# Performance work log

Measured on AMD Instinct MI355X. Metric: run time of the kernel, lower is better.

Reference implementation:

```python
import jax, jax.numpy as jnp
import numpy as np

B, S, D, H = 2, 2048, 2048, 16
DH = D // H  # 128


def _rope(x, cos, sin):
    # Faithful to the source: x is (B, H, S, Dh) (already transposed), and the
    # original apply_rotary_emb slices freqs_cis[:, :H, :] and broadcasts over
    # the S axis -> rotation angle depends on head index (source quirk).
    h = x.shape[1]
    c = cos[:, :h, :][:, :, None, :]  # (1, H, 1, Dh/2)
    s = sin[:, :h, :][:, :, None, :]
    half = x.shape[-1] // 2
    re, im = x[..., :half], x[..., half:]
    return jnp.concatenate([re * c - im * s, re * s + im * c], axis=-1)


def setup_inputs() -> dict:
    key = jax.random.key(0)
    k0, k1, k2 = jax.random.split(key, 3)
    x = jax.random.normal(k0, (B, S, D), jnp.float32)
    Wqkv = jax.random.normal(k1, (D, 3 * D), jnp.float32) / np.float32(np.sqrt(D))
    bqkv = jnp.zeros((3 * D,), jnp.float32)
    Wout = jax.random.normal(k2, (D, D), jnp.float32) / np.float32(np.sqrt(D))
    bout = jnp.zeros((D,), jnp.float32)
    # standard RoPE frequency table, stored as cos/sin (unit-modulus complex)
    inv_freq = 1.0 / (10000.0 ** (np.arange(0, DH // 2, dtype=np.float32) / (DH // 2)))
    ang = np.outer(np.arange(S, dtype=np.float32), inv_freq)  # (S, Dh/2)
    freqs_cos = jnp.asarray(np.cos(ang)[None], jnp.float32)   # (1, S, Dh/2)
    freqs_sin = jnp.asarray(np.sin(ang)[None], jnp.float32)
    mask = jnp.triu(jnp.ones((S, S), bool), 1)[None, None]    # causal, True = masked
    return {"x": x, "Wqkv": Wqkv, "bqkv": bqkv, "Wout": Wout, "bout": bout,
            "freqs_cos": freqs_cos, "freqs_sin": freqs_sin, "mask": mask}


def reference(x, Wqkv, bqkv, Wout, bout, freqs_cos, freqs_sin, mask):
    b, s, d = x.shape
    scale = DH ** (-0.5)
    qkv = x @ Wqkv + bqkv                                   # (B, S, 3D)
    q, k, v = jnp.split(qkv, 3, axis=-1)
    to_heads = lambda t: t.reshape(b, s, H, DH).transpose(0, 2, 1, 3)  # (B,H,S,Dh)
    q, k, v = to_heads(q), to_heads(k), to_heads(v)
    q = _rope(q, freqs_cos, freqs_sin)
    k = _rope(k, freqs_cos, freqs_sin)
    scores = jnp.einsum('bhqd,bhkd->bhqk', q, k) * scale
    scores = jnp.where(mask, -jnp.inf, scores)
    p = jax.nn.softmax(scores, axis=-1)                     # dropout p=0 (eval)
    out = jnp.einsum('bhqk,bhkd->bhqd', p, v)
    out = out.transpose(0, 2, 1, 3).reshape(b, s, d)
    return out @ Wout + bout
```

## Files before the change

kernel.cpp:

```cpp
#include <hip/hip_runtime.h>

#define S_ 2048
#define D_ 2048
#define H_ 16
#define DH_ 128

typedef __attribute__((ext_vector_type(8))) short short8;
typedef __attribute__((ext_vector_type(4))) float f32x4;
typedef __attribute__((ext_vector_type(8))) unsigned short ushort8;
typedef __attribute__((ext_vector_type(4))) unsigned short ushort4v;

__device__ __forceinline__ unsigned short f2bf(float f) {
  unsigned int u;
  __builtin_memcpy(&u, &f, 4);
  unsigned int lsb = (u >> 16) & 1u;
  u += 0x7fffu + lsb;
  return (unsigned short)(u >> 16);
}

__device__ __forceinline__ void gload_lds16(const void* g, void* l) {
  __builtin_amdgcn_global_load_lds(
      (const __attribute__((address_space(1))) unsigned int*)g,
      (__attribute__((address_space(3))) unsigned int*)l, 16, 0, 0);
}

template <int N> __device__ __forceinline__ void vmwait() {
  if constexpr (N == 8)      asm volatile("s_waitcnt vmcnt(8)" ::: "memory");
  else if constexpr (N == 6) asm volatile("s_waitcnt vmcnt(6)" ::: "memory");
  else if constexpr (N == 4) asm volatile("s_waitcnt vmcnt(4)" ::: "memory");
  else if constexpr (N == 3) asm volatile("s_waitcnt vmcnt(3)" ::: "memory");
  else if constexpr (N == 2) asm volatile("s_waitcnt vmcnt(2)" ::: "memory");
  else                       asm volatile("s_waitcnt vmcnt(0)" ::: "memory");
}

#define FENCE_ asm volatile("" ::: "memory")
#define BAR_ { FENCE_; __builtin_amdgcn_s_barrier(); FENCE_; }

__device__ __forceinline__ void prep_w_tile(
    const float* __restrict__ W, const float* __restrict__ cosb,
    const float* __restrict__ sinb, unsigned short* __restrict__ WT,
    int Nw, int rot_limit, int kt, int nt, float (*tile)[129]) {
  const int t = threadIdx.x;
#pragma unroll
  for (int i = 0; i < 4; ++i) {
    int q = i * 256 + t;
    int kl = q >> 5, cq = q & 31;
    float4 v = *(const float4*)(W + (size_t)(kt + kl) * Nw + nt + cq * 4);
    tile[kl][cq * 4 + 0] = v.x; tile[kl][cq * 4 + 1] = v.y;
    tile[kl][cq * 4 + 2] = v.z; tile[kl][cq * 4 + 3] = v.w;
  }
  __syncthreads();
  const bool rot = nt < rot_limit;
#pragma unroll
  for (int i = 0; i < 16; ++i) {
    int f = i * 256 + t;
    int kl = f & 31, nl = f >> 5;
    int ng = nt + nl;
    float val;
    if (rot) {
      int i0 = nl & 63;
      int h = (ng & 2047) >> 7;
      float c = cosb[h * 64 + i0], sn = sinb[h * 64 + i0];
      float re = tile[kl][i0], im = tile[kl][i0 + 64];
      val = (nl < 64) ? (re * c - im * sn) : (re * sn + im * c);
    } else {
      val = tile[kl][nl];
    }
    WT[(size_t)ng * 2048 + kt + kl] = f2bf(val);
  }
}

__global__ void k_prep(const float* __restrict__ x, unsigned short* __restrict__ xb,
                       const float* __restrict__ Wqkv, const float* __restrict__ Wout,
                       const float* __restrict__ cosb, const float* __restrict__ sinb,
                       unsigned short* __restrict__ wqkvT, unsigned short* __restrict__ woutT) {
  __shared__ float tile[32][129];
  const int bid = blockIdx.x;
  if (bid < 4096) {
    int idx = bid * 256 + threadIdx.x;
    const float4* xv = (const float4*)x;
    float4 a = xv[(size_t)idx * 2];
    float4 b = xv[(size_t)idx * 2 + 1];
    ushort8 o;
    o[0] = f2bf(a.x); o[1] = f2bf(a.y); o[2] = f2bf(a.z); o[3] = f2bf(a.w);
    o[4] = f2bf(b.x); o[5] = f2bf(b.y); o[6] = f2bf(b.z); o[7] = f2bf(b.w);
    *(ushort8*)(xb + (size_t)idx * 8) = o;
  } else if (bid < 7168) {
    int b2 = bid - 4096;
    prep_w_tile(Wqkv, cosb, sinb, wqkvT, 6144, 4096,
                (b2 & 63) * 32, (b2 >> 6) * 128, tile);
  } else {
    int b3 = bid - 7168;
    prep_w_tile(Wout, cosb, sinb, woutT, 2048, 0,
                (b3 & 63) * 32, (b3 >> 6) * 128, tile);
  }
}

template <int NF, int MODE>
__global__ __launch_bounds__(512, 2) void k_ms(
    const unsigned short* __restrict__ A, const unsigned short* __restrict__ Bt,
    const float* __restrict__ bias,
    unsigned short* __restrict__ Qb, unsigned short* __restrict__ Kb,
    unsigned short* __restrict__ Vt, float* __restrict__ Co) {
  constexpr int BN = NF * 64;
  constexpr int NT = 32;
  constexpr int BBASE = 65536;
  constexpr int BSZ = BN * 128;
  __shared__ unsigned char lds[BBASE + 3 * BSZ];

  const int tid = threadIdx.x, l = tid & 63, w = tid >> 6;
  const int wm = w >> 2, wn = w & 3;
  const int bid = blockIdx.x;
  int tmi = (bid & 1) * 8 + ((bid >> 3) & 7);
  int tni;
  if constexpr (NF == 3) tni = ((bid >> 1) & 3) * 8 + (bid >> 6);
  else                   tni = ((bid >> 1) & 3) * 4 + (bid >> 6);
  const int tm = tmi * 256;
  const int tn = tni * BN;

  const int sslot = (l & 7) ^ (l >> 3);
  const unsigned short* aB = A + (size_t)(tm + (l >> 3)) * 2048 + sslot * 8;
  const unsigned short* bB = Bt + (size_t)(tn + (l >> 3)) * 2048 + sslot * 8;
  const int xg = ((l >> 4) ^ (l & 7)) << 4;
  const int afo = (wm * 128 + (l & 15)) * 128 + xg;
  const int bfo = (wn * (NF * 16) + (l & 15)) * 128 + xg;

  f32x4 acc[8][NF] = {};
  short8 af[8], bf[2 * NF];

#define SAF_(ab_, u_) {                                                         \
  _Pragma("unroll") for (int i_ = 0; i_ < 4; ++i_) {                            \
    int c_ = w + i_ * 8;                                                        \
    gload_lds16(aB + (size_t)(c_ * 8) * 2048 + (u_) * 64,                       \
                lds + (ab_) + c_ * 1024); } }
#define SBF_(bs_, u_) {                                                         \
  _Pragma("unroll") for (int i_ = 0; i_ < NF; ++i_) {                           \
    int c_ = w + i_ * 8;                                                        \
    gload_lds16(bB + (size_t)(c_ * 8) * 2048 + (u_) * 64,                       \
                lds + (bs_) + c_ * 1024); } }
#define RDA2_(ab_, mh_) {                                                       \
  _Pragma("unroll") for (int m_ = 0; m_ < 4; ++m_) {                            \
    unsigned a_ = (ab_) + afo + ((mh_) * 4 + m_) * 2048;                        \
    af[m_]     = *(const short8*)(lds + a_);                                    \
    af[4 + m_] = *(const short8*)(lds + (a_ ^ 64)); } }
#define RDB2_(bb_) {                                                            \
  _Pragma("unroll") for (int n_ = 0; n_ < NF; ++n_) {                           \
    unsigned a_ = (bb_) + bfo + n_ * 2048;                                      \
    bf[n_]      = *(const short8*)(lds + a_);                                   \
    bf[NF + n_] = *(const short8*)(lds + (a_ ^ 64)); } }
#define MMF_(mh_) { __builtin_amdgcn_s_setprio(1);                              \
  _Pragma("unroll") for (int kk_ = 0; kk_ < 2; ++kk_)                           \
  _Pragma("unroll") for (int m_ = 0; m_ < 4; ++m_)                              \
  _Pragma("unroll") for (int n_ = 0; n_ < NF; ++n_)                             \
    acc[(mh_) * 4 + m_][n_] = __builtin_amdgcn_mfma_f32_16x16x32_bf16(          \
        af[kk_ * 4 + m_], bf[kk_ * NF + n_], acc[(mh_) * 4 + m_][n_], 0, 0, 0); \
  __builtin_amdgcn_s_setprio(0); }

  SAF_(0u, 0); SBF_(BBASE, 0); SBF_(BBASE + BSZ, 1);
  vmwait<NF>(); BAR_;

  int bcur = 0, bstg = 2;
#pragma unroll 1
  for (int v = 0; v < NT; ++v) {
    const unsigned ab = (unsigned)(v & 1) * 32768u;
    const unsigned an = (unsigned)((v + 1) & 1) * 32768u;
    const unsigned bb = BBASE + (unsigned)bcur * BSZ;
    const unsigned bs = BBASE + (unsigned)bstg * BSZ;
    RDB2_(bb);
    RDA2_(ab, 0);
    if (v + 1 < NT) SAF_(an, v + 1);
    MMF_(0);
    RDA2_(ab, 1);
    if (v + 2 < NT) SBF_(bs, v + 2);
    MMF_(1);
    if (v < NT - 2) { vmwait<NF>(); } else { vmwait<0>(); }
    BAR_;
    bcur = (bcur == 2) ? 0 : bcur + 1;
    bstg = (bstg == 2) ? 0 : bstg + 1;
  }
#undef SAF_
#undef SBF_
#undef RDA2_
#undef RDB2_
#undef MMF_

  const int ln = l & 15, rb4 = (l >> 4) << 2;
#pragma unroll
  for (int m = 0; m < 8; ++m) {
    int rbase = tm + wm * 128 + m * 16 + rb4;
#pragma unroll
    for (int n = 0; n < NF; ++n) {
      int colg = tn + wn * (NF * 16) + n * 16 + ln;
      float bv = bias[colg];
      if constexpr (MODE == 0) {
        int reg = colg >> 11;
        int h = (colg & 2047) >> 7, dh = colg & 127;
        if (reg == 2) {
          int b = rbase >> 11, s = rbase & 2047;
          ushort4v o;
#pragma unroll
          for (int j = 0; j < 4; ++j) o[j] = f2bf(acc[m][n][j] + bv);
          *(ushort4v*)(Vt + ((size_t)(b * H_ + h) * DH_ + dh) * S_ + s) = o;
        } else {
#pragma unroll
          for (int j = 0; j < 4; ++j) {
            int r = rbase + j;
            int b = r >> 11, s = r & 2047;
            size_t off = ((size_t)(b * H_ + h) * S_ + s) * DH_ + dh;
            float v = acc[m][n][j] + bv;
            if (reg == 0) Qb[off] = f2bf(v * 0.08838834764831845f);
            else Kb[off] = f2bf(v);
          }
        }
      } else {
#pragma unroll
        for (int j = 0; j < 4; ++j)
          Co[(size_t)(rbase + j) * 2048 + colg] = acc[m][n][j] + bv;
      }
    }
  }
}

__global__ __launch_bounds__(512) void k_attn(
    const unsigned short* __restrict__ Qb, const unsigned short* __restrict__ Kb,
    const unsigned short* __restrict__ Vt, unsigned short* __restrict__ Ob) {
  __shared__ unsigned short kls[2][8192];
  __shared__ unsigned short vls[2][8192];
  __shared__ unsigned short pls[8192];
  const int t = threadIdx.x, l = t & 63, w = t >> 6;
  const int id = blockIdx.x;
  const int pairi = id >> 5, bh = id & 31;
  const int b = bh >> 4, h = bh & 15;
  const int lq = l & 15, lg = l >> 4;
  const int rb = lg << 2;
  const unsigned short* Qp = Qb + (size_t)bh * S_ * DH_;
  const unsigned short* Kp = Kb + (size_t)bh * S_ * DH_;
  const unsigned short* Vp = Vt + (size_t)bh * DH_ * S_;

#pragma unroll 1
  for (int half = 0; half < 2; ++half) {
    const int qt = half ? (15 - pairi) : pairi;
    const int qb = qt * 128;
    const int qrow = qb + w * 16 + lq;
    const int nkv = 2 * qt + 2;

    short8 qf[4];
#pragma unroll
    for (int c = 0; c < 4; ++c)
      qf[c] = *(const short8*)(Qp + (size_t)qrow * 128 + c * 32 + lg * 8);

    f32x4 o[8] = {};
    float m = -1e30f, lsum = 0.f;

#pragma unroll
    for (int i = 0; i < 2; ++i) {
      int cid = w + i * 8;
      int krow = cid * 4 + (l >> 4);
      int kslot = (l & 15) ^ (krow & 7);
      gload_lds16(Kp + (size_t)krow * 128 + kslot * 8, &kls[0][cid * 512]);
      int vrow = cid * 8 + (l >> 3);
      int vslot = (l & 7) ^ (vrow & 7);
      gload_lds16(Vp + (size_t)vrow * S_ + vslot * 8, &vls[0][cid * 512]);
    }
    __syncthreads();

#pragma unroll 1
    for (int kvt = 0; kvt < nkv; ++kvt) {
      const int kvb = kvt * 64;
      const int cur = kvt & 1;

      if (kvt + 1 < nkv) {
        const int kvb2 = kvb + 64;
#pragma unroll
        for (int i = 0; i < 2; ++i) {
          int cid = w + i * 8;
          int krow = cid * 4 + (l >> 4);
          int kslot = (l & 15) ^ (krow & 7);
          gload_lds16(Kp + (size_t)(kvb2 + krow) * 128 + kslot * 8,
                      &kls[cur ^ 1][cid * 512]);
          int vrow = cid * 8 + (l >> 3);
          int vslot = (l & 7) ^ (vrow & 7);
          gload_lds16(Vp + (size_t)vrow * S_ + kvb2 + vslot * 8,
                      &vls[cur ^ 1][cid * 512]);
        }
      }

      f32x4 sc[4];
      __builtin_amdgcn_s_setprio(1);
#pragma unroll
      for (int nb = 0; nb < 4; ++nb) {
        f32x4 sacc = {};
#pragma unroll
        for (int c = 0; c < 4; ++c) {
          int row = nb * 16 + lq;
          int off = (c * 64 + (lg * 16)) ^ ((row & 7) << 4);
          short8 kf = *(const short8*)((const char*)kls[cur] + row * 256 + off);
          sacc = __builtin_amdgcn_mfma_f32_16x16x32_bf16(kf, qf[c], sacc, 0, 0, 0);
        }
        sc[nb] = sacc;
      }
      __builtin_amdgcn_s_setprio(0);

      float xs[4][4];
      float xm = -1e30f;
      const bool diag = (kvb + 63) > (qb + w * 16);
#pragma unroll
      for (int nb = 0; nb < 4; ++nb)
#pragma unroll
        for (int r = 0; r < 4; ++r) {
          float x = sc[nb][r];
          if (diag && (kvb + nb * 16 + rb + r > qrow)) x = -1e30f;
          xs[nb][r] = x;
          xm = fmaxf(xm, x);
        }
      xm = fmaxf(xm, __shfl_xor(xm, 16));
      xm = fmaxf(xm, __shfl_xor(xm, 32));

      if (__any(xm > m + 8.f)) {
        float nm = fmaxf(m, xm);
        float f = __expf(m - nm);
        m = nm; lsum *= f;
        float fj[4];
#pragma unroll
        for (int j = 0; j < 4; ++j) fj[j] = __shfl(f, (l & 48) | (rb + j));
#pragma unroll
        for (int d = 0; d < 8; ++d) {
          o[d][0] *= fj[0]; o[d][1] *= fj[1]; o[d][2] *= fj[2]; o[d][3] *= fj[3];
        }
      }
      float s = 0.f;
#pragma unroll
      for (int nb = 0; nb < 4; ++nb)
#pragma unroll
        for (int r = 0; r < 4; ++r) {
          float p = __expf(xs[nb][r] - m);
          xs[nb][r] = p;
          s += p;
        }
      s += __shfl_xor(s, 16);
      s += __shfl_xor(s, 32);
      lsum += s;

#pragma unroll
      for (int nb = 0; nb < 4; ++nb) {
        ushort4v pw;
#pragma unroll
        for (int r = 0; r < 4; ++r) pw[r] = f2bf(xs[nb][r]);
        *(ushort4v*)((char*)pls + w * 2048 + lq * 128 +
                     ((nb * 32 + lg * 8) ^ ((lq & 7) << 4))) = pw;
      }

      __builtin_amdgcn_s_setprio(1);
#pragma unroll
      for (int kc = 0; kc < 2; ++kc) {
        short8 pa = *(const short8*)((const char*)pls + w * 2048 + lq * 128 +
                                     ((kc * 64 + lg * 16) ^ ((lq & 7) << 4)));
#pragma unroll
        for (int d = 0; d < 8; ++d) {
          int vrow = d * 16 + lq;
          int voff = (kc * 64 + (lg * 16)) ^ ((vrow & 7) << 4);
          short8 vf = *(const short8*)((const char*)vls[cur] + vrow * 128 + voff);
          o[d] = __builtin_amdgcn_mfma_f32_16x16x32_bf16(pa, vf, o[d], 0, 0, 0);
        }
      }
      __builtin_amdgcn_s_setprio(0);
      __syncthreads();
    }

    float inv = 1.f / lsum;
    float invj[4];
#pragma unroll
    for (int j = 0; j < 4; ++j) invj[j] = __shfl(inv, (l & 48) | (rb + j));
#pragma unroll
    for (int d = 0; d < 8; ++d) {
#pragma unroll
      for (int j = 0; j < 4; ++j) {
        int s = qb + w * 16 + rb + j;
        int col = h * 128 + d * 16 + lq;
        Ob[((size_t)(b * S_ + s)) * D_ + col] = f2bf(o[d][j] * invj[j]);
      }
    }
  }
}

extern "C" void kernel_launch(void* const* d_in, const int* in_sizes, int n_in,
                              void* d_out, int out_size, void* d_ws, size_t ws_size,
                              hipStream_t stream) {
  const float* x    = (const float*)d_in[0];
  const float* Wqkv = (const float*)d_in[1];
  const float* bqkv = (const float*)d_in[2];
  const float* Wout = (const float*)d_in[3];
  const float* bout = (const float*)d_in[4];
  const float* fcos = (const float*)d_in[5];
  const float* fsin = (const float*)d_in[6];
  float* out = (float*)d_out;

  char* ws = (char*)d_ws;
  unsigned short* xbf   = (unsigned short*)(ws);
  unsigned short* wqkvT = (unsigned short*)(ws + 16777216);
  unsigned short* woutT = (unsigned short*)(ws + 41943040);
  unsigned short* Qb    = (unsigned short*)(ws + 50331648);
  unsigned short* Kb    = Qb + 8388608;
  unsigned short* Vtb   = Kb + 8388608;
  unsigned short* Ob    = xbf;

  hipLaunchKernelGGL(k_prep, dim3(8192), dim3(256), 0, stream,
                     x, xbf, Wqkv, Wout, fcos, fsin, wqkvT, woutT);
  hipLaunchKernelGGL((k_ms<3, 0>), dim3(512), dim3(512), 0, stream,
                     xbf, wqkvT, bqkv, Qb, Kb, Vtb, (float*)nullptr);
  hipLaunchKernelGGL(k_attn, dim3(256), dim3(512), 0, stream, Qb, Kb, Vtb, Ob);
  hipLaunchKernelGGL((k_ms<2, 1>), dim3(256), dim3(512), 0, stream,
                     Ob, woutT, bout, (unsigned short*)nullptr,
                     (unsigned short*)nullptr, (unsigned short*)nullptr, out);
}
```

Baseline: 238.4 us.

## Replace QKV projection GEMM with smaller-tile 128x96 kernel and XCD-aware mapping

Adds a dedicated QKV GEMM kernel that uses 256-thread blocks with 128x96 output tiles, a double-buffered A tile and a triple-buffered B tile in LDS, and a block-to-tile mapping that groups neighbouring tiles on the same XCD. It launches 2048 smaller blocks instead of 512 large k_ms blocks, aiming for better occupancy, load balance and L2 locality. The epilogue writes Q (pre-scaled), K and transposed V directly. Smaller tiles lower arithmetic intensity and the Q/K stores are scalar 2-byte writes, which may cost bandwidth.

```diff
diff --git a/kernel.cpp b/kernel.cpp
--- a/kernel.cpp
+++ b/kernel.cpp
@@ -93,6 +93,120 @@
     int b3 = bid - 7168;
     prep_w_tile(Wout, cosb, sinb, woutT, 2048, 0,
                 (b3 & 63) * 32, (b3 >> 6) * 128, tile);
+  }
+}
+
+__global__ __launch_bounds__(256, 2) void k_g1(
+    const unsigned short* __restrict__ A, const unsigned short* __restrict__ Bt,
+    const float* __restrict__ bias,
+    unsigned short* __restrict__ Qb, unsigned short* __restrict__ Kb,
+    unsigned short* __restrict__ Vt) {
+  constexpr int NT = 32;
+  constexpr int ABASE = 0;
+  constexpr int BBASE = 32768;
+  __shared__ unsigned char lds[69632];
+
+  const int tid = threadIdx.x, l = tid & 63, w = tid >> 6;
+  const int wm = w >> 1, wn = w & 1;
+  const int bid = blockIdx.x;
+  const int xcd = bid & 7, local = bid >> 3;
+  const int tmi = (xcd & 1) * 16 + (local & 15);
+  const int tni = (xcd >> 1) * 16 + (local >> 4);
+  const int tm = tmi * 128;
+  const int tn = tni * 96;
+
+  const int sslot = (l & 7) ^ (l >> 3);
+  const unsigned short* aB = A + (size_t)(tm + (l >> 3)) * 2048 + sslot * 8;
+  const unsigned short* bB = Bt + (size_t)(tn + (l >> 3)) * 2048 + sslot * 8;
+  const int xg = ((l >> 4) ^ (l & 7)) << 4;
+  const int afo = (wm * 64 + (l & 15)) * 128 + xg;
+  const int bfo = (wn * 48 + (l & 15)) * 128 + xg;
+
+  f32x4 acc[4][3] = {};
+  short8 af[8], bf[6];
+
+#define SAF_(ab_, u_) {                                                         \
+  _Pragma("unroll") for (int i_ = 0; i_ < 4; ++i_) {                            \
+    int c_ = w + i_ * 4;                                                        \
+    gload_lds16(aB + (size_t)(c_ * 8) * 2048 + (u_) * 64,                       \
+                lds + (ab_) + c_ * 1024); } }
+#define SBF_(bs_, u_) {                                                         \
+  _Pragma("unroll") for (int i_ = 0; i_ < 3; ++i_) {                            \
+    int c_ = w + i_ * 4;                                                        \
+    gload_lds16(bB + (size_t)(c_ * 8) * 2048 + (u_) * 64,                       \
+                lds + (bs_) + c_ * 1024); } }
+#define RDA2_(ab_) {                                                            \
+  _Pragma("unroll") for (int m_ = 0; m_ < 4; ++m_) {                            \
+    unsigned a_ = (ab_) + afo + m_ * 2048;                                      \
+    af[m_]     = *(const short8*)(lds + a_);                                    \
+    af[4 + m_] = *(const short8*)(lds + (a_ ^ 64)); } }
+#define RDB2_(bb_) {                                                            \
+  _Pragma("unroll") for (int n_ = 0; n_ < 3; ++n_) {                            \
+    unsigned a_ = (bb_) + bfo + n_ * 2048;                                      \
+    bf[n_]     = *(const short8*)(lds + a_);                                    \
+    bf[3 + n_] = *(const short8*)(lds + (a_ ^ 64)); } }
+#define MMF_() { __builtin_amdgcn_s_setprio(1);                                 \
+  _Pragma("unroll") for (int kk_ = 0; kk_ < 2; ++kk_)                           \
+  _Pragma("unroll") for (int m_ = 0; m_ < 4; ++m_)                              \
+  _Pragma("unroll") for (int n_ = 0; n_ < 3; ++n_)                              \
+    acc[m_][n_] = __builtin_amdgcn_mfma_f32_16x16x32_bf16(                      \
+        af[kk_ * 4 + m_], bf[kk_ * 3 + n_], acc[m_][n_], 0, 0, 0);              \
+  __builtin_amdgcn_s_setprio(0); }
+
+  SAF_(ABASE, 0); SBF_(BBASE, 0); SBF_(BBASE + 12288, 1);
+  vmwait<3>(); BAR_;
+
+  int bcur = 0, bstg = 2;
+#pragma unroll 1
+  for (int v = 0; v < NT; ++v) {
+    const unsigned ab = ABASE + (unsigned)(v & 1) * 16384u;
+    const unsigned an = ABASE + (unsigned)((v + 1) & 1) * 16384u;
+    const unsigned bb = BBASE + (unsigned)bcur * 12288u;
+    const unsigned bs = BBASE + (unsigned)bstg * 12288u;
+    RDB2_(bb);
+    RDA2_(ab);
+    if (v + 1 < NT) SAF_(an, v + 1);
+    if (v + 2 < NT) SBF_(bs, v + 2);
+    MMF_();
+    if (v < NT - 2) { vmwait<3>(); } else { vmwait<0>(); }
+    BAR_;
+    bcur = (bcur == 2) ? 0 : bcur + 1;
+    bstg = (bstg == 2) ? 0 : bstg + 1;
+  }
+#undef SAF_
+#undef SBF_
+#undef RDA2_
+#undef RDB2_
+#undef MMF_
+
+  const int ln = l & 15, rb4 = (l >> 4) << 2;
+#pragma unroll
+  for (int m = 0; m < 4; ++m) {
+    int rbase = tm + wm * 64 + m * 16 + rb4;
+#pragma unroll
+    for (int n = 0; n < 3; ++n) {
+      int colg = tn + wn * 48 + n * 16 + ln;
+      float bv = bias[colg];
+      int reg = colg >> 11;
+      int h = (colg & 2047) >> 7, dh = colg & 127;
+      if (reg == 2) {
+        int b = rbase >> 11, s = rbase & 2047;
+        ushort4v o;
+#pragma unroll
+        for (int j = 0; j < 4; ++j) o[j] = f2bf(acc[m][n][j] + bv);
+        *(ushort4v*)(Vt + ((size_t)(b * H_ + h) * DH_ + dh) * S_ + s) = o;
+      } else {
+#pragma unroll
+        for (int j = 0; j < 4; ++j) {
+          int r = rbase + j;
+          int b = r >> 11, s = r & 2047;
+          size_t off = ((size_t)(b * H_ + h) * S_ + s) * DH_ + dh;
+          float v = acc[m][n][j] + bv;
+          if (reg == 0) Qb[off] = f2bf(v * 0.08838834764831845f);
+          else Kb[off] = f2bf(v);
+        }
+      }
+    }
   }
 }
 
@@ -406,8 +520,8 @@
 
   hipLaunchKernelGGL(k_prep, dim3(8192), dim3(256), 0, stream,
                      x, xbf, Wqkv, Wout, fcos, fsin, wqkvT, woutT);
-  hipLaunchKernelGGL((k_ms<3, 0>), dim3(512), dim3(512), 0, stream,
-                     xbf, wqkvT, bqkv, Qb, Kb, Vtb, (float*)nullptr);
+  hipLaunchKernelGGL(k_g1, dim3(2048), dim3(256), 0, stream,
+                     xbf, wqkvT, bqkv, Qb, Kb, Vtb);
   hipLaunchKernelGGL(k_attn, dim3(256), dim3(512), 0, stream, Qb, Kb, Vtb, Ob);
   hipLaunchKernelGGL((k_ms<2, 1>), dim3(256), dim3(512), 0, stream,
                      Ob, woutT, bout, (unsigned short*)nullptr,
```

Measured after the change: 261.4 us. 1.1x slower.

## Use 32x32 MFMA tiles and process both causal query tiles concurrently

Applied to the files above, without the earlier changes.

The attention kernel switches from 16x16x32 to 32x32x16 bf16 MFMA, giving each wave 32 query rows. Instead of handling the paired query tiles one after the other, waves 0-3 take tile p and waves 4-7 take tile 15-p, all sharing one K/V streaming loop over the longer range. Waves whose tile is already past the diagonal skip compute but keep joining the barriers. This cuts LDS fragment reads per FLOP and removes the second prologue and serial pass, at the cost of more accumulator registers and some idle waves late in the loop.

```diff
diff --git a/kernel.cpp b/kernel.cpp
--- a/kernel.cpp
+++ b/kernel.cpp
@@ -7,6 +7,7 @@
 
 typedef __attribute__((ext_vector_type(8))) short short8;
 typedef __attribute__((ext_vector_type(4))) float f32x4;
+typedef __attribute__((ext_vector_type(16))) float f32x16;
 typedef __attribute__((ext_vector_type(8))) unsigned short ushort8;
 typedef __attribute__((ext_vector_type(4))) unsigned short ushort4v;
 
@@ -226,161 +227,165 @@
     const unsigned short* __restrict__ Vt, unsigned short* __restrict__ Ob) {
   __shared__ unsigned short kls[2][8192];
   __shared__ unsigned short vls[2][8192];
-  __shared__ unsigned short pls[8192];
+  __shared__ unsigned short pls[16384];
   const int t = threadIdx.x, l = t & 63, w = t >> 6;
   const int id = blockIdx.x;
-  const int pairi = id >> 5, bh = id & 31;
+  const int p = id >> 5, bh = id & 31;
   const int b = bh >> 4, h = bh & 15;
-  const int lq = l & 15, lg = l >> 4;
-  const int rb = lg << 2;
+  const int lq = l & 31, lh = l >> 5;
   const unsigned short* Qp = Qb + (size_t)bh * S_ * DH_;
   const unsigned short* Kp = Kb + (size_t)bh * S_ * DH_;
   const unsigned short* Vp = Vt + (size_t)bh * DH_ * S_;
 
+  const int tile = (w < 4) ? p : (15 - p);
+  const int qbw = tile * 128 + (w & 3) * 32;
+  const int qrow = qbw + lq;
+  const int nkv = 32 - 2 * p;
+
+  short8 qf[8];
+#pragma unroll
+  for (int c = 0; c < 8; ++c)
+    qf[c] = *(const short8*)(Qp + (size_t)qrow * 128 + c * 16 + lh * 8);
+
+  f32x16 o[4] = {};
+  float m = -1e30f, lsum = 0.f;
+
+#pragma unroll
+  for (int i = 0; i < 2; ++i) {
+    int cid = w + i * 8;
+    int krow = cid * 4 + (l >> 4);
+    int kslot = (l & 15) ^ (krow & 7);
+    gload_lds16(Kp + (size_t)krow * 128 + kslot * 8, &kls[0][cid * 512]);
+    int vrow = cid * 8 + (l >> 3);
+    int vslot = (l & 7) ^ (vrow & 7);
+    gload_lds16(Vp + (size_t)vrow * S_ + vslot * 8, &vls[0][cid * 512]);
+  }
+  __syncthreads();
+
 #pragma unroll 1
-  for (int half = 0; half < 2; ++half) {
-    const int qt = half ? (15 - pairi) : pairi;
-    const int qb = qt * 128;
-    const int qrow = qb + w * 16 + lq;
-    const int nkv = 2 * qt + 2;
-
-    short8 qf[4];
-#pragma unroll
-    for (int c = 0; c < 4; ++c)
-      qf[c] = *(const short8*)(Qp + (size_t)qrow * 128 + c * 32 + lg * 8);
-
-    f32x4 o[8] = {};
-    float m = -1e30f, lsum = 0.f;
-
-#pragma unroll
-    for (int i = 0; i < 2; ++i) {
-      int cid = w + i * 8;
-      int krow = cid * 4 + (l >> 4);
-      int kslot = (l & 15) ^ (krow & 7);
-      gload_lds16(Kp + (size_t)krow * 128 + kslot * 8, &kls[0][cid * 512]);
-      int vrow = cid * 8 + (l >> 3);
-      int vslot = (l & 7) ^ (vrow & 7);
-      gload_lds16(Vp + (size_t)vrow * S_ + vslot * 8, &vls[0][cid * 512]);
+  for (int kvt = 0; kvt < nkv; ++kvt) {
+    const int kvb = kvt * 64;
+    const int cur = kvt & 1;
+
+    if (kvt + 1 < nkv) {
+      const int kvb2 = kvb + 64;
+#pragma unroll
+      for (int i = 0; i < 2; ++i) {
+        int cid = w + i * 8;
+        int krow = cid * 4 + (l >> 4);
+        int kslot = (l & 15) ^ (krow & 7);
+        gload_lds16(Kp + (size_t)(kvb2 + krow) * 128 + kslot * 8,
+                    &kls[cur ^ 1][cid * 512]);
+        int vrow = cid * 8 + (l >> 3);
+        int vslot = (l & 7) ^ (vrow & 7);
+        gload_lds16(Vp + (size_t)vrow * S_ + kvb2 + vslot * 8,
+                    &vls[cur ^ 1][cid * 512]);
+      }
     }
-    __syncthreads();
-
-#pragma unroll 1
-    for (int kvt = 0; kvt < nkv; ++kvt) {
-      const int kvb = kvt * 64;
-      const int cur = kvt & 1;
-
-      if (kvt + 1 < nkv) {
-        const int kvb2 = kvb + 64;
-#pragma unroll
-        for (int i = 0; i < 2; ++i) {
-          int cid = w + i * 8;
-          int krow = cid * 4 + (l >> 4);
-          int kslot = (l & 15) ^ (krow & 7);
-          gload_lds16(Kp + (size_t)(kvb2 + krow) * 128 + kslot * 8,
-                      &kls[cur ^ 1][cid * 512]);
-          int vrow = cid * 8 + (l >> 3);
-          int vslot = (l & 7) ^ (vrow & 7);
-          gload_lds16(Vp + (size_t)vrow * S_ + kvb2 + vslot * 8,
-                      &vls[cur ^ 1][cid * 512]);
-        }
-      }
-
-      f32x4 sc[4];
+
+    if (kvb <= qbw + 31) {
+      f32x16 sc0 = {}, sc1 = {};
       __builtin_amdgcn_s_setprio(1);
 #pragma unroll
-      for (int nb = 0; nb < 4; ++nb) {
-        f32x4 sacc = {};
-#pragma unroll
-        for (int c = 0; c < 4; ++c) {
-          int row = nb * 16 + lq;
-          int off = (c * 64 + (lg * 16)) ^ ((row & 7) << 4);
-          short8 kf = *(const short8*)((const char*)kls[cur] + row * 256 + off);
-          sacc = __builtin_amdgcn_mfma_f32_16x16x32_bf16(kf, qf[c], sacc, 0, 0, 0);
-        }
-        sc[nb] = sacc;
+      for (int c = 0; c < 8; ++c) {
+        int col = (c * 32 + lh * 16) ^ ((l & 7) << 4);
+        short8 kf0 = *(const short8*)((const char*)kls[cur] + lq * 256 + col);
+        short8 kf1 = *(const short8*)((const char*)kls[cur] + (32 + lq) * 256 + col);
+        sc0 = __builtin_amdgcn_mfma_f32_32x32x16_bf16(kf0, qf[c], sc0, 0, 0, 0);
+        sc1 = __builtin_amdgcn_mfma_f32_32x32x16_bf16(kf1, qf[c], sc1, 0, 0, 0);
       }
       __builtin_amdgcn_s_setprio(0);
 
-      float xs[4][4];
+      float xs[2][16];
+      const bool diag = (kvb + 63) > qbw;
+#pragma unroll
+      for (int r = 0; r < 16; ++r) { xs[0][r] = sc0[r]; xs[1][r] = sc1[r]; }
+      if (diag) {
+#pragma unroll
+        for (int kt = 0; kt < 2; ++kt)
+#pragma unroll
+          for (int r = 0; r < 16; ++r) {
+            int kg = kvb + kt * 32 + (r & 3) + 8 * (r >> 2) + 4 * lh;
+            if (kg > qrow) xs[kt][r] = -1e30f;
+          }
+      }
       float xm = -1e30f;
-      const bool diag = (kvb + 63) > (qb + w * 16);
-#pragma unroll
-      for (int nb = 0; nb < 4; ++nb)
-#pragma unroll
-        for (int r = 0; r < 4; ++r) {
-          float x = sc[nb][r];
-          if (diag && (kvb + nb * 16 + rb + r > qrow)) x = -1e30f;
-          xs[nb][r] = x;
-          xm = fmaxf(xm, x);
-        }
-      xm = fmaxf(xm, __shfl_xor(xm, 16));
+#pragma unroll
+      for (int kt = 0; kt < 2; ++kt)
+#pragma unroll
+        for (int r = 0; r < 16; ++r) xm = fmaxf(xm, xs[kt][r]);
       xm = fmaxf(xm, __shfl_xor(xm, 32));
 
       if (__any(xm > m + 8.f)) {
         float nm = fmaxf(m, xm);
         float f = __expf(m - nm);
         m = nm; lsum *= f;
-        float fj[4];
-#pragma unroll
-        for (int j = 0; j < 4; ++j) fj[j] = __shfl(f, (l & 48) | (rb + j));
-#pragma unroll
-        for (int d = 0; d < 8; ++d) {
-          o[d][0] *= fj[0]; o[d][1] *= fj[1]; o[d][2] *= fj[2]; o[d][3] *= fj[3];
+        float fj[16];
+#pragma unroll
+        for (int r = 0; r < 16; ++r)
+          fj[r] = __shfl(f, (r & 3) + 8 * (r >> 2) + 4 * lh);
+#pragma unroll
+        for (int dt = 0; dt < 4; ++dt)
+#pragma unroll
+          for (int r = 0; r < 16; ++r) o[dt][r] *= fj[r];
+      }
+      float s = 0.f;
+#pragma unroll
+      for (int kt = 0; kt < 2; ++kt)
+#pragma unroll
+        for (int r = 0; r < 16; ++r) {
+          float pv = __expf(xs[kt][r] - m);
+          xs[kt][r] = pv;
+          s += pv;
         }
-      }
-      float s = 0.f;
-#pragma unroll
-      for (int nb = 0; nb < 4; ++nb)
-#pragma unroll
-        for (int r = 0; r < 4; ++r) {
-          float p = __expf(xs[nb][r] - m);
-          xs[nb][r] = p;
-          s += p;
-        }
-      s += __shfl_xor(s, 16);
       s += __shfl_xor(s, 32);
       lsum += s;
 
 #pragma unroll
-      for (int nb = 0; nb < 4; ++nb) {
-        ushort4v pw;
-#pragma unroll
-        for (int r = 0; r < 4; ++r) pw[r] = f2bf(xs[nb][r]);
-        *(ushort4v*)((char*)pls + w * 2048 + lq * 128 +
-                     ((nb * 32 + lg * 8) ^ ((lq & 7) << 4))) = pw;
-      }
-
+      for (int kt = 0; kt < 2; ++kt)
+#pragma unroll
+        for (int g2 = 0; g2 < 4; ++g2) {
+          ushort4v pw;
+#pragma unroll
+          for (int j = 0; j < 4; ++j) pw[j] = f2bf(xs[kt][g2 * 4 + j]);
+          *(ushort4v*)((char*)pls + w * 4096 + lq * 128 +
+                       (((kt * 64 + g2 * 16) ^ ((l & 7) << 4)) + lh * 8)) = pw;
+        }
+
+      short8 pa[4];
+#pragma unroll
+      for (int ks = 0; ks < 4; ++ks)
+        pa[ks] = *(const short8*)((const char*)pls + w * 4096 + lq * 128 +
+                                  ((ks * 32 + lh * 16) ^ ((l & 7) << 4)));
       __builtin_amdgcn_s_setprio(1);
 #pragma unroll
-      for (int kc = 0; kc < 2; ++kc) {
-        short8 pa = *(const short8*)((const char*)pls + w * 2048 + lq * 128 +
-                                     ((kc * 64 + lg * 16) ^ ((lq & 7) << 4)));
-#pragma unroll
-        for (int d = 0; d < 8; ++d) {
-          int vrow = d * 16 + lq;
-          int voff = (kc * 64 + (lg * 16)) ^ ((vrow & 7) << 4);
-          short8 vf = *(const short8*)((const char*)vls[cur] + vrow * 128 + voff);
-          o[d] = __builtin_amdgcn_mfma_f32_16x16x32_bf16(pa, vf, o[d], 0, 0, 0);
+      for (int dt = 0; dt < 4; ++dt) {
+#pragma unroll
+        for (int ks = 0; ks < 4; ++ks) {
+          int vrow = dt * 32 + lq;
+          short8 vf = *(const short8*)((const char*)vls[cur] + vrow * 128 +
+                                       ((ks * 32 + lh * 16) ^ ((vrow & 7) << 4)));
+          o[dt] = __builtin_amdgcn_mfma_f32_32x32x16_bf16(pa[ks], vf, o[dt], 0, 0, 0);
         }
       }
       __builtin_amdgcn_s_setprio(0);
-      __syncthreads();
     }
-
-    float inv = 1.f / lsum;
-    float invj[4];
-#pragma unroll
-    for (int j = 0; j < 4; ++j) invj[j] = __shfl(inv, (l & 48) | (rb + j));
-#pragma unroll
-    for (int d = 0; d < 8; ++d) {
-#pragma unroll
-      for (int j = 0; j < 4; ++j) {
-        int s = qb + w * 16 + rb + j;
-        int col = h * 128 + d * 16 + lq;
-        Ob[((size_t)(b * S_ + s)) * D_ + col] = f2bf(o[d][j] * invj[j]);
-      }
+    __syncthreads();
+  }
+
+  float inv = 1.f / lsum;
+  float invj[16];
+#pragma unroll
+  for (int r = 0; r < 16; ++r)
+    invj[r] = __shfl(inv, (r & 3) + 8 * (r >> 2) + 4 * lh);
+#pragma unroll
+  for (int dt = 0; dt < 4; ++dt)
+#pragma unroll
+    for (int r = 0; r < 16; ++r) {
+      int srow = qbw + (r & 3) + 8 * (r >> 2) + 4 * lh;
+      int col = h * 128 + dt * 32 + lq;
+      Ob[((size_t)(b * S_ + srow)) * D_ + col] = f2bf(o[dt][r] * invj[r]);
     }
-  }
 }
 
 extern "C" void kernel_launch(void* const* d_in, const int* in_sizes, int n_in,
```

Result: no change. 236.0 us (-1.0%).
